# Kernel tuning notes

Measured on AMD Instinct MI355X. Metric: run time of the kernel, lower is better.

Reference implementation:

```python
import jax, jax.numpy as jnp
import numpy as np

G = 8            # grid_size
G2 = G * G       # total_grid_size = 64
NS = 2.0         # neighborhood_size
H = 64           # h_dim
A = 1024         # bottleneck_dim == attention_dim
S = 32           # number of sequences
N = 64           # pedestrians per sequence
P = 4096         # scene boundary points per sequence (down_samples)
B = S * N        # total batch = 2048


def setup_inputs() -> dict:
    key = jax.random.key(0)
    ks = jax.random.split(key, 16)
    starts = jnp.arange(S, dtype=jnp.int32) * N
    seq_start_end = jnp.stack([starts, starts + N], axis=1)  # (S, 2) uniform groups
    return {
        "h_states": jax.random.normal(ks[0], (1, B, H), jnp.float32),
        "end_pos": jax.random.normal(ks[1], (B, 2), jnp.float32),
        "rel_pos": jax.random.normal(ks[2], (B, 2), jnp.float32) * 0.1,
        "scene_info": jax.random.normal(ks[3], (S, P, 2), jnp.float32),
        # Attention_Decoder params (soft attention over G2 grid cells, encoder_dim=1)
        "W_enc": jax.random.normal(ks[4], (1, A), jnp.float32) * 0.05,
        "b_enc": jnp.zeros((A,), jnp.float32),
        "W_dec": jax.random.normal(ks[5], (H, A), jnp.float32) * 0.05,
        "b_dec": jnp.zeros((A,), jnp.float32),
        "w_full": jax.random.normal(ks[6], (A, 1), jnp.float32) * 0.05,
        "b_full": jnp.zeros((1,), jnp.float32),
        "W_out": jax.random.normal(ks[7], (1 + H + 4, A), jnp.float32) * 0.05,  # [ctx, h, embed_info]
        "b_out": jnp.zeros((A,), jnp.float32),
        # mlp_pool: Linear(A, A) + BatchNorm1d + ReLU
        "W_mlp": jax.random.normal(ks[8], (A, A), jnp.float32) * 0.05,
        "b_mlp": jnp.zeros((A,), jnp.float32),
        "gamma": jnp.ones((A,), jnp.float32),
        "beta": jnp.zeros((A,), jnp.float32),
        "seq_start_end": seq_start_end,
    }


def _occupancy(end_pos, scene_info, num_seqs, peds, grid_size, ns):
    """Vectorized per-pedestrian grid-cell binning + scatter-add occupancy.
    end_pos: (num_seqs*peds, 2), scene_info: (num_seqs, P, 2) -> (B, G2)."""
    g2 = grid_size * grid_size
    b = num_seqs * peds
    ep = end_pos.reshape(num_seqs, peds, 1, 2)
    sx = scene_info[:, None, :, 0]  # (S, 1, P)
    sy = scene_info[:, None, :, 1]
    tl_x = ep[..., 0] - ns / 2
    tl_y = ep[..., 1] + ns / 2
    br_x = ep[..., 0] + ns / 2
    br_y = ep[..., 1] - ns / 2
    cell_x = jnp.floor((sx - tl_x) / ns * grid_size)   # (S, N, P)
    cell_y = jnp.floor((tl_y - sy) / ns * grid_size)
    cell = (cell_x + cell_y * grid_size).astype(jnp.int32)
    # point is out-of-bound if outside the ped's neighborhood box (matches torch mask)
    oob = (sx >= br_x) | (sx <= tl_x) | (sy >= tl_y) | (sy <= br_y)
    ped = jnp.arange(b, dtype=jnp.int32).reshape(num_seqs, peds, 1)
    # torch scatters masked points into slot 0 then drops it; we use one dump slot at the end
    idx = jnp.where(oob, b * g2, ped * g2 + cell)      # (S, N, P)
    counts = jax.ops.segment_sum(
        jnp.ones(idx.size, jnp.float32), idx.reshape(-1), num_segments=b * g2 + 1)
    return counts[:-1].reshape(b, g2)


def reference(h_states, end_pos, rel_pos, scene_info,
              W_enc, b_enc, W_dec, b_dec, w_full, b_full,
              W_out, b_out, W_mlp, b_mlp, gamma, beta, seq_start_end):
    num_seqs = seq_start_end.shape[0]
    b = end_pos.shape[0]
    peds = b // num_seqs
    occ = _occupancy(end_pos, scene_info, num_seqs, peds, G, NS)   # (B, G2)
    enc = occ[..., None]                                           # (B, G2, 1)
    h = h_states.reshape(b, -1)                                    # (B, H)
    embed_info = jnp.concatenate([end_pos, rel_pos], axis=1)       # (B, 4)
    # soft attention over the G2 grid cells conditioned on the decoder hidden state
    att = jax.nn.relu(enc @ W_enc + b_enc + (h @ W_dec + b_dec)[:, None, :])  # (B, G2, A)
    e = (att @ w_full)[..., 0] + b_full                            # (B, G2)
    alpha = jax.nn.softmax(e, axis=1)
    ctx = jnp.sum(alpha[..., None] * enc, axis=1)                  # (B, 1)
    pool = jnp.concatenate([ctx, h, embed_info], axis=1) @ W_out + b_out  # (B, A)
    # mlp_pool: Linear -> BatchNorm1d (training stats, biased var) -> ReLU
    y = pool @ W_mlp + b_mlp
    mu = jnp.mean(y, axis=0)
    var = jnp.mean((y - mu) ** 2, axis=0)
    y = gamma * (y - mu) * jax.lax.rsqrt(var + 1e-5) + beta
    return jax.nn.relu(y)
```

## Files before the change

### kernel.cpp

```cpp
#include <hip/hip_runtime.h>
#include <hip/hip_bf16.h>


#define NG2  64
#define NPTS 4096

typedef unsigned short ushort_t;
typedef __attribute__((ext_vector_type(8))) short bf16x8;
typedef __attribute__((ext_vector_type(4))) float f32x4;

struct PrepPtrs { const void* p[16]; };

__device__ __forceinline__ float bf2f(ushort_t u) {
  return __uint_as_float(((unsigned int)u) << 16);
}
__device__ __forceinline__ ushort_t f2bf(float f) {
  __hip_bfloat16 b = __float2bfloat16(f);
  return *reinterpret_cast<ushort_t*>(&b);
}
__device__ __forceinline__ float lde(const void* p, size_t i, int fl) {
  return fl ? bf2f(((const ushort_t*)p)[i]) : ((const float*)p)[i];
}
__device__ __forceinline__ int block_flag(const ushort_t* h) {
  __shared__ int bad_sh;
  if (threadIdx.x == 0) bad_sh = 0;
  __syncthreads();
  float v = bf2f(h[threadIdx.x & 255]);
  if (!(fabsf(v) <= 1e4f)) atomicOr(&bad_sh, 1);
  __syncthreads();
  return (bad_sh == 0) ? 1 : 0;
}

__device__ __forceinline__ void tp_body(const void* in, int fl, int job,
                                        int Kin, int Kpad, ushort_t* out) {
  __shared__ ushort_t t[32][40];
  int n0 = (job & 31) * 32, k0 = (job >> 5) * 32;
  int r = threadIdx.x >> 3, c4 = (threadIdx.x & 7) * 4;
  ushort4 v = make_ushort4(0, 0, 0, 0);
  if (k0 + r < Kin) {
    size_t off = (size_t)(k0 + r) * 1024 + n0 + c4;
    if (fl) {
      v = *(const ushort4*)((const ushort_t*)in + off);
    } else {
      float4 f = *(const float4*)((const float*)in + off);
      v = make_ushort4(f2bf(f.x), f2bf(f.y), f2bf(f.z), f2bf(f.w));
    }
  }
  *(ushort4*)(&t[r][c4]) = v;
  __syncthreads();
  int n = threadIdx.x >> 3, kk = (threadIdx.x & 7) * 4;
  ushort4 o = make_ushort4(t[kk][n], t[kk + 1][n], t[kk + 2][n], t[kk + 3][n]);
  *(ushort4*)(out + (size_t)(n0 + n) * Kpad + k0 + kk) = o;
}

__global__ __launch_bounds__(256) void k_prep(PrepPtrs ptrs,
                                              float* __restrict__ conv,
                                              ushort_t* __restrict__ hbf,
                                              ushort_t* __restrict__ WdecT,
                                              ushort_t* __restrict__ WoutT,
                                              ushort_t* __restrict__ WmlpT,
                                              ushort_t* __restrict__ Xcat0,
                                              float* __restrict__ occ,
                                              float* __restrict__ stats) {
  int b = blockIdx.x;
  int fl = block_flag((const ushort_t*)ptrs.p[0]);
  if (b < 9) {
    int idx = (b * 256 + threadIdx.x) * 4;
    int seg = idx >> 10, off = idx & 1023;
    float4 o;
    if (fl) {
      const unsigned int* src = (const unsigned int*)ptrs.p[7 + seg];
      uint2 u = *(const uint2*)(src + (off >> 1));
      o.x = __uint_as_float((u.x & 0xFFFFu) << 16);
      o.y = __uint_as_float(u.x & 0xFFFF0000u);
      o.z = __uint_as_float((u.y & 0xFFFFu) << 16);
      o.w = __uint_as_float(u.y & 0xFFFF0000u);
    } else {
      o = *(const float4*)((const float*)ptrs.p[7 + seg] + off);
    }
    *(float4*)(conv + idx) = o;
  } else if (b < 137) {
    int i = (b - 9) * 256 + threadIdx.x;
    if (fl) {
      ((ushort4*)hbf)[i] = ((const ushort4*)ptrs.p[0])[i];
    } else {
      float4 f = ((const float4*)ptrs.p[0])[i];
      ((ushort4*)hbf)[i] = make_ushort4(f2bf(f.x), f2bf(f.y), f2bf(f.z), f2bf(f.w));
    }
  } else if (b < 201) {
    tp_body(ptrs.p[1], fl, b - 137, 64, 64, WdecT);
  } else if (b < 297) {
    const void* wout1 = fl ? (const void*)((const ushort_t*)ptrs.p[2] + 1024)
                           : (const void*)((const float*)ptrs.p[2] + 1024);
    tp_body(wout1, fl, b - 201, 68, 96, WoutT);
  } else if (b < 1321) {
    tp_body(ptrs.p[3], fl, b - 297, 1024, 1024, WmlpT);
  } else if (b < 1513) {
    int flat = (b - 1321) * 256 + threadIdx.x;
    int e4 = flat * 4;
    int r = e4 / 96, c = e4 - r * 96;
    ushort4 v = make_ushort4(0, 0, 0, 0);
    if (c < 64) {
      if (fl) v = *(const ushort4*)((const ushort_t*)ptrs.p[0] + r * 64 + c);
      else {
        float4 f = *(const float4*)((const float*)ptrs.p[0] + r * 64 + c);
        v = make_ushort4(f2bf(f.x), f2bf(f.y), f2bf(f.z), f2bf(f.w));
      }
    } else if (c == 64) {
      v.x = f2bf(lde(ptrs.p[4], 2 * r, fl));
      v.y = f2bf(lde(ptrs.p[4], 2 * r + 1, fl));
      v.z = f2bf(lde(ptrs.p[5], 2 * r, fl));
      v.w = f2bf(lde(ptrs.p[5], 2 * r + 1, fl));
    }
    *(ushort4*)(Xcat0 + e4) = v;
  } else if (b < 3561) {
    int i = b - 1513;
    int s = i >> 6;
    __shared__ float cnth[NG2];
    if (threadIdx.x < NG2) cnth[threadIdx.x] = 0.0f;
    __syncthreads();
    float ex = lde(ptrs.p[4], 2 * i, fl), ey = lde(ptrs.p[4], 2 * i + 1, fl);
    float tlx = ex - 1.0f, tly = ey + 1.0f, brx = ex + 1.0f, bry = ey - 1.0f;
    const void* scn = ptrs.p[6];
    for (int p = threadIdx.x; p < NPTS; p += 256) {
      size_t o2 = (size_t)s * NPTS * 2 + 2 * p;
      float sx = lde(scn, o2, fl), sy = lde(scn, o2 + 1, fl);
      bool oob = (sx >= brx) || (sx <= tlx) || (sy >= tly) || (sy <= bry);
      if (!oob) {
        int cx = (int)floorf((sx - tlx) * 0.5f * 8.0f);
        int cy = (int)floorf((tly - sy) * 0.5f * 8.0f);
        int cell = cx + cy * 8;
        if (cell >= 0 && cell < NG2) atomicAdd(&cnth[cell], 1.0f);
      }
    }
    __syncthreads();
    if (threadIdx.x < NG2) occ[i * NG2 + threadIdx.x] = cnth[threadIdx.x];
  } else {
#pragma unroll
    for (int k = 0; k < 8; k++) stats[threadIdx.x + 256 * k] = 0.0f;
  }
}

template <int K, int EPI>
__device__ __forceinline__ void mgemm_body(
    ushort_t* As, ushort_t* Bs, int m0, int n0,
    const ushort_t* __restrict__ A, int lda,
    const ushort_t* __restrict__ BT, int ldb,
    const float* __restrict__ bias1, const float* __restrict__ bias2,
    ushort_t* __restrict__ outb, float* __restrict__ outf) {
  int tid = threadIdx.x;
  int wave = tid >> 6, lane = tid & 63, l15 = lane & 15, kg = lane >> 4;
  f32x4 acc[4][2] = {};
  int ar = tid >> 2, ag = tid & 3;
  int aswz = ag ^ ((ar >> 1) & 3);
  for (int k0 = 0; k0 < K; k0 += 32) {
    uint4 av = *(const uint4*)(A + (size_t)(m0 + ar) * lda + k0 + ag * 8);
    *(uint4*)(&As[ar * 32 + aswz * 8]) = av;
#pragma unroll
    for (int i = 0; i < 2; i++) {
      int c = tid + i * 256;
      int br = c >> 2, bg = c & 3;
      int bswz = bg ^ ((br >> 1) & 3);
      uint4 bv = *(const uint4*)(BT + (size_t)(n0 + br) * ldb + k0 + bg * 8);
      *(uint4*)(&Bs[br * 32 + bswz * 8]) = bv;
    }
    __syncthreads();
    bf16x8 af[4], bfr[2];
#pragma unroll
    for (int mt = 0; mt < 4; mt++) {
      int row = mt * 16 + l15;
      int swz = kg ^ ((row >> 1) & 3);
      af[mt] = *(const bf16x8*)(&As[row * 32 + swz * 8]);
    }
#pragma unroll
    for (int nt = 0; nt < 2; nt++) {
      int row = wave * 32 + nt * 16 + l15;
      int swz = kg ^ ((row >> 1) & 3);
      bfr[nt] = *(const bf16x8*)(&Bs[row * 32 + swz * 8]);
    }
#pragma unroll
    for (int mt = 0; mt < 4; mt++)
#pragma unroll
      for (int nt = 0; nt < 2; nt++)
        acc[mt][nt] = __builtin_amdgcn_mfma_f32_16x16x32_bf16(af[mt], bfr[nt], acc[mt][nt], 0, 0, 0);
    __syncthreads();
  }
#pragma unroll
  for (int nt = 0; nt < 2; nt++) {
    int col = n0 + wave * 32 + nt * 16 + l15;
    float bsum = (EPI == 0) ? (bias1[col] + bias2[col]) : bias1[col];
#pragma unroll
    for (int mt = 0; mt < 4; mt++) {
#pragma unroll
      for (int r = 0; r < 4; r++) {
        int rowm = m0 + mt * 16 + kg * 4 + r;
        float v = acc[mt][nt][r] + bsum;
        if (EPI == 3) outf[(size_t)rowm * 1024 + col] = v;
        else outb[(size_t)rowm * 1024 + col] = f2bf(v);
      }
    }
  }
}

__global__ __launch_bounds__(256) void k_gemm2(
    const ushort_t* __restrict__ hbf, const ushort_t* __restrict__ WdecT,
    const float* __restrict__ benc, const float* __restrict__ bdec,
    ushort_t* __restrict__ hd_out,
    const ushort_t* __restrict__ Xcat0, const ushort_t* __restrict__ WoutT,
    const float* __restrict__ bout, float* __restrict__ P1) {
  __shared__ ushort_t As[64 * 32];
  __shared__ ushort_t Bs[128 * 32];
  int m0 = blockIdx.x * 64, n0 = blockIdx.y * 128;
  if (blockIdx.z == 0)
    mgemm_body<64, 0>(As, Bs, m0, n0, hbf, 64, WdecT, 64, benc, bdec, hd_out, nullptr);
  else
    mgemm_body<96, 3>(As, Bs, m0, n0, Xcat0, 96, WoutT, 96, bout, nullptr, nullptr, P1);
}

__global__ __launch_bounds__(256) void k_ygemm(
    const ushort_t* __restrict__ A, const ushort_t* __restrict__ BT,
    const float* __restrict__ bias1, ushort_t* __restrict__ outb,
    float* __restrict__ stats) {
  __shared__ ushort_t As[64 * 32];
  __shared__ ushort_t Bs[64 * 32];
  int m0 = blockIdx.x * 64, n0 = blockIdx.y * 64;
  int tid = threadIdx.x;
  int wave = tid >> 6, lane = tid & 63, l15 = lane & 15, kg = lane >> 4;
  f32x4 acc[4] = {};
  int ar = tid >> 2, ag = tid & 3;
  int aswz = ag ^ ((ar >> 1) & 3);
  for (int k0 = 0; k0 < 1024; k0 += 32) {
    uint4 av = *(const uint4*)(A + (size_t)(m0 + ar) * 1024 + k0 + ag * 8);
    *(uint4*)(&As[ar * 32 + aswz * 8]) = av;
    {
      int br = tid >> 2, bg = tid & 3;
      int bswz = bg ^ ((br >> 1) & 3);
      uint4 bv = *(const uint4*)(BT + (size_t)(n0 + br) * 1024 + k0 + bg * 8);
      *(uint4*)(&Bs[br * 32 + bswz * 8]) = bv;
    }
    __syncthreads();
    bf16x8 af[4], bfr;
#pragma unroll
    for (int mt = 0; mt < 4; mt++) {
      int row = mt * 16 + l15;
      int swz = kg ^ ((row >> 1) & 3);
      af[mt] = *(const bf16x8*)(&As[row * 32 + swz * 8]);
    }
    {
      int row = wave * 16 + l15;
      int swz = kg ^ ((row >> 1) & 3);
      bfr = *(const bf16x8*)(&Bs[row * 32 + swz * 8]);
    }
#pragma unroll
    for (int mt = 0; mt < 4; mt++)
      acc[mt] = __builtin_amdgcn_mfma_f32_16x16x32_bf16(af[mt], bfr, acc[mt], 0, 0, 0);
    __syncthreads();
  }
  int col = n0 + wave * 16 + l15;
  float bsum = bias1[col];
  float s1 = 0.0f, s2 = 0.0f;
#pragma unroll
  for (int mt = 0; mt < 4; mt++) {
#pragma unroll
    for (int r = 0; r < 4; r++) {
      int rowm = m0 + mt * 16 + kg * 4 + r;
      float v = acc[mt][r] + bsum;
      outb[(size_t)rowm * 1024 + col] = f2bf(v);
      s1 += v; s2 = fmaf(v, v, s2);
    }
  }
  s1 += __shfl_down(s1, 16); s2 += __shfl_down(s2, 16);
  s1 += __shfl_down(s1, 32); s2 += __shfl_down(s2, 32);
  if (lane < 16) {
    atomicAdd(&stats[col], s1);
    atomicAdd(&stats[1024 + col], s2);
  }
}

__global__ __launch_bounds__(256) void k_ectx(
    const float* __restrict__ occ,
    const float* __restrict__ Wenc, const float* __restrict__ wfull,
    const float* __restrict__ w0, const float* __restrict__ P1,
    const ushort_t* __restrict__ hd, ushort_t* __restrict__ pool) {
  int wave = threadIdx.x >> 6, lane = threadIdx.x & 63;
  int p = blockIdx.x * 4 + wave;
  __shared__ float occ_sh[4][64];
  occ_sh[wave][lane] = occ[p * 64 + lane];
  float hdv[16], we[16], wf[16];
#pragma unroll
  for (int j = 0; j < 16; j++) {
    int a = lane + j * 64;
    hdv[j] = bf2f(hd[(size_t)p * 1024 + a]);
    we[j] = Wenc[a];
    wf[j] = wfull[a];
  }
  float e_mine = 0.0f;
  for (int g = 0; g < 64; g++) {
    float c = occ_sh[wave][g];
    float s = 0.0f;
#pragma unroll
    for (int j = 0; j < 16; j++)
      s += fmaxf(fmaf(c, we[j], hdv[j]), 0.0f) * wf[j];
#pragma unroll
    for (int off = 32; off > 0; off >>= 1) s += __shfl_xor(s, off);
    if (lane == g) e_mine = s;
  }
  float m = e_mine;
#pragma unroll
  for (int off = 32; off > 0; off >>= 1) m = fmaxf(m, __shfl_xor(m, off));
  float xe = __expf(e_mine - m);
  float den = xe;
#pragma unroll
  for (int off = 32; off > 0; off >>= 1) den += __shfl_xor(den, off);
  float cp = xe * occ_sh[wave][lane];
#pragma unroll
  for (int off = 32; off > 0; off >>= 1) cp += __shfl_xor(cp, off);
  float ctx = cp / den;
#pragma unroll
  for (int j = 0; j < 16; j++) {
    int a = lane + j * 64;
    pool[(size_t)p * 1024 + a] = f2bf(fmaf(ctx, w0[a], P1[(size_t)p * 1024 + a]));
  }
}

__global__ void k_norm(const ushort_t* __restrict__ y_mf,
                       const float* __restrict__ stats,
                       const float* __restrict__ gamma, const float* __restrict__ beta,
                       const ushort_t* __restrict__ hsrc, void* __restrict__ out) {
  int fl = block_flag(hsrc);
  int idx = (blockIdx.x * 256 + threadIdx.x) * 4;
  int col = idx & 1023;
  float vv[4];
#pragma unroll
  for (int j = 0; j < 4; j++) vv[j] = bf2f(y_mf[idx + j]);
  float4 s1 = *(const float4*)(stats + col);
  float4 s2 = *(const float4*)(stats + 1024 + col);
  float4 gm = *(const float4*)(gamma + col);
  float4 bt = *(const float4*)(beta + col);
  const float ib = 1.0f / 2048.0f;
  float m1[4] = {s1.x, s1.y, s1.z, s1.w};
  float m2[4] = {s2.x, s2.y, s2.z, s2.w};
  float gg[4] = {gm.x, gm.y, gm.z, gm.w};
  float bb[4] = {bt.x, bt.y, bt.z, bt.w};
  float o[4];
#pragma unroll
  for (int j = 0; j < 4; j++) {
    float mu = m1[j] * ib;
    float var = fmaf(-mu, mu, m2[j] * ib);
    o[j] = fmaxf(fmaf(gg[j] * (vv[j] - mu), rsqrtf(var + 1e-5f), bb[j]), 0.0f);
  }
  if (fl) {
    ushort4 ov = make_ushort4(f2bf(o[0]), f2bf(o[1]), f2bf(o[2]), f2bf(o[3]));
    *(ushort4*)((ushort_t*)out + idx) = ov;
  } else {
    *(float4*)((float*)out + idx) = make_float4(o[0], o[1], o[2], o[3]);
  }
}

extern "C" void kernel_launch(void* const* d_in, const int* in_sizes, int n_in,
                              void* d_out, int out_size, void* d_ws, size_t ws_size,
                              hipStream_t stream) {
  float* ws = (float*)d_ws;
  float* conv   = ws;
  float* c_Wenc = conv + 0;
  float* c_benc = conv + 1024;
  float* c_bdec = conv + 2048;
  float* c_wful = conv + 3072;
  float* c_bout = conv + 4096;
  float* c_bmlp = conv + 5120;
  float* c_gam  = conv + 6144;
  float* c_bet  = conv + 7168;
  float* c_w0   = conv + 8192;
  float* occ    = ws + 9216;
  float* stats  = ws + 140288;
  float* P1     = ws + 142336;
  ushort_t* u0    = (ushort_t*)(ws + 2239488);
  ushort_t* hbf   = u0;
  ushort_t* WdecT = u0 + 131072;
  ushort_t* WoutT = u0 + 196608;
  ushort_t* WmlpT = u0 + 294912;
  ushort_t* Xcat0 = u0 + 1343488;
  ushort_t* y_mf  = u0 + 1540096;
  ushort_t* hd_bf   = (ushort_t*)d_out;
  ushort_t* pool_mf = (ushort_t*)d_out;

  PrepPtrs ptrs;
  ptrs.p[0] = d_in[0];
  ptrs.p[1] = d_in[6];
  ptrs.p[2] = d_in[10];
  ptrs.p[3] = d_in[12];
  ptrs.p[4] = d_in[1];
  ptrs.p[5] = d_in[2];
  ptrs.p[6] = d_in[3];
  ptrs.p[7]  = d_in[4];
  ptrs.p[8]  = d_in[5];
  ptrs.p[9]  = d_in[7];
  ptrs.p[10] = d_in[8];
  ptrs.p[11] = d_in[11];
  ptrs.p[12] = d_in[13];
  ptrs.p[13] = d_in[14];
  ptrs.p[14] = d_in[15];
  ptrs.p[15] = d_in[10];

  k_prep<<<3562, 256, 0, stream>>>(ptrs, conv, hbf, WdecT, WoutT, WmlpT,
                                   Xcat0, occ, stats);

  k_gemm2<<<dim3(32, 8, 2), 256, 0, stream>>>(hbf, WdecT, c_benc, c_bdec, hd_bf,
                                              Xcat0, WoutT, c_bout, P1);

  k_ectx<<<512, 256, 0, stream>>>(occ, c_Wenc, c_wful, c_w0, P1, hd_bf, pool_mf);

  k_ygemm<<<dim3(32, 16), 256, 0, stream>>>(pool_mf, WmlpT, c_bmlp, y_mf, stats);

  k_norm<<<2048, 256, 0, stream>>>(y_mf, stats, c_gam, c_bet,
                                   (const ushort_t*)d_in[0], d_out);
}
```

Before: 162.4 us.

## Rebalance prep kernel: larger per-block work for copy, transpose, and occupancy binning

Shrinks the prep kernel grid from 3562 to 1194 blocks by giving each block more work. The h_states conversion now handles 8 elements per thread. The W_mlp transpose uses dedicated 64x64 LDS tiles with padded rows in place of the generic tp_body. Occupancy binning runs one pedestrian per wavefront with per-wave LDS histograms and vectorized scene-point loads. The aim is to cut block launch and scheduling overhead and get better load widths, at the cost of less parallelism per pedestrian in the binning loop.

```diff
diff --git a/kernel.cpp b/kernel.cpp
--- a/kernel.cpp
+++ b/kernel.cpp
@@ -79,24 +79,52 @@
       o = *(const float4*)((const float*)ptrs.p[7 + seg] + off);
     }
     *(float4*)(conv + idx) = o;
-  } else if (b < 137) {
+  } else if (b < 73) {
     int i = (b - 9) * 256 + threadIdx.x;
     if (fl) {
-      ((ushort4*)hbf)[i] = ((const ushort4*)ptrs.p[0])[i];
+      ((uint4*)hbf)[i] = ((const uint4*)ptrs.p[0])[i];
     } else {
-      float4 f = ((const float4*)ptrs.p[0])[i];
-      ((ushort4*)hbf)[i] = make_ushort4(f2bf(f.x), f2bf(f.y), f2bf(f.z), f2bf(f.w));
-    }
-  } else if (b < 201) {
-    tp_body(ptrs.p[1], fl, b - 137, 64, 64, WdecT);
-  } else if (b < 297) {
+      float4 f0 = ((const float4*)ptrs.p[0])[2 * i];
+      float4 f1 = ((const float4*)ptrs.p[0])[2 * i + 1];
+      ((ushort4*)hbf)[2 * i]     = make_ushort4(f2bf(f0.x), f2bf(f0.y), f2bf(f0.z), f2bf(f0.w));
+      ((ushort4*)hbf)[2 * i + 1] = make_ushort4(f2bf(f1.x), f2bf(f1.y), f2bf(f1.z), f2bf(f1.w));
+    }
+  } else if (b < 137) {
+    tp_body(ptrs.p[1], fl, b - 73, 64, 64, WdecT);
+  } else if (b < 233) {
     const void* wout1 = fl ? (const void*)((const ushort_t*)ptrs.p[2] + 1024)
                            : (const void*)((const float*)ptrs.p[2] + 1024);
-    tp_body(wout1, fl, b - 201, 68, 96, WoutT);
-  } else if (b < 1321) {
-    tp_body(ptrs.p[3], fl, b - 297, 1024, 1024, WmlpT);
-  } else if (b < 1513) {
-    int flat = (b - 1321) * 256 + threadIdx.x;
+    tp_body(wout1, fl, b - 137, 68, 96, WoutT);
+  } else if (b < 489) {
+    __shared__ ushort_t t64[64 * 68];
+    int job = b - 233;
+    int n0 = (job & 15) * 64, k0 = (job >> 4) * 64;
+    const void* in = ptrs.p[3];
+#pragma unroll
+    for (int i = 0; i < 4; i++) {
+      int chunk = threadIdx.x + i * 256;
+      int r = chunk >> 4, c4 = (chunk & 15) * 4;
+      ushort4 v;
+      size_t off = (size_t)(k0 + r) * 1024 + n0 + c4;
+      if (fl) {
+        v = *(const ushort4*)((const ushort_t*)in + off);
+      } else {
+        float4 f = *(const float4*)((const float*)in + off);
+        v = make_ushort4(f2bf(f.x), f2bf(f.y), f2bf(f.z), f2bf(f.w));
+      }
+      *(ushort4*)(&t64[r * 68 + c4]) = v;
+    }
+    __syncthreads();
+#pragma unroll
+    for (int i = 0; i < 4; i++) {
+      int chunk = threadIdx.x + i * 256;
+      int n = chunk >> 4, k4 = (chunk & 15) * 4;
+      ushort4 o = make_ushort4(t64[(k4 + 0) * 68 + n], t64[(k4 + 1) * 68 + n],
+                               t64[(k4 + 2) * 68 + n], t64[(k4 + 3) * 68 + n]);
+      *(ushort4*)(WmlpT + (size_t)(n0 + n) * 1024 + k0 + k4) = o;
+    }
+  } else if (b < 681) {
+    int flat = (b - 489) * 256 + threadIdx.x;
     int e4 = flat * 4;
     int r = e4 / 96, c = e4 - r * 96;
     ushort4 v = make_ushort4(0, 0, 0, 0);
@@ -113,28 +141,37 @@
       v.w = f2bf(lde(ptrs.p[5], 2 * r + 1, fl));
     }
     *(ushort4*)(Xcat0 + e4) = v;
-  } else if (b < 3561) {
-    int i = b - 1513;
+  } else if (b < 1193) {
+    int wave = threadIdx.x >> 6, lane = threadIdx.x & 63;
+    int i = (b - 681) * 4 + wave;
     int s = i >> 6;
-    __shared__ float cnth[NG2];
-    if (threadIdx.x < NG2) cnth[threadIdx.x] = 0.0f;
+    __shared__ float cnth[4][NG2];
+    cnth[wave][lane] = 0.0f;
     __syncthreads();
     float ex = lde(ptrs.p[4], 2 * i, fl), ey = lde(ptrs.p[4], 2 * i + 1, fl);
     float tlx = ex - 1.0f, tly = ey + 1.0f, brx = ex + 1.0f, bry = ey - 1.0f;
     const void* scn = ptrs.p[6];
-    for (int p = threadIdx.x; p < NPTS; p += 256) {
-      size_t o2 = (size_t)s * NPTS * 2 + 2 * p;
-      float sx = lde(scn, o2, fl), sy = lde(scn, o2 + 1, fl);
+    for (int p = lane; p < NPTS; p += 64) {
+      size_t pi = (size_t)s * NPTS + p;
+      float sx, sy;
+      if (fl) {
+        unsigned int u = ((const unsigned int*)scn)[pi];
+        sx = __uint_as_float((u & 0xFFFFu) << 16);
+        sy = __uint_as_float(u & 0xFFFF0000u);
+      } else {
+        float2 f = *((const float2*)scn + pi);
+        sx = f.x; sy = f.y;
+      }
       bool oob = (sx >= brx) || (sx <= tlx) || (sy >= tly) || (sy <= bry);
       if (!oob) {
         int cx = (int)floorf((sx - tlx) * 0.5f * 8.0f);
         int cy = (int)floorf((tly - sy) * 0.5f * 8.0f);
         int cell = cx + cy * 8;
-        if (cell >= 0 && cell < NG2) atomicAdd(&cnth[cell], 1.0f);
+        if (cell >= 0 && cell < NG2) atomicAdd(&cnth[wave][cell], 1.0f);
       }
     }
     __syncthreads();
-    if (threadIdx.x < NG2) occ[i * NG2 + threadIdx.x] = cnth[threadIdx.x];
+    occ[(size_t)i * NG2 + lane] = cnth[wave][lane];
   } else {
 #pragma unroll
     for (int k = 0; k < 8; k++) stats[threadIdx.x + 256 * k] = 0.0f;
@@ -402,7 +439,7 @@
   ptrs.p[14] = d_in[15];
   ptrs.p[15] = d_in[10];
 
-  k_prep<<<3562, 256, 0, stream>>>(ptrs, conv, hbf, WdecT, WoutT, WmlpT,
+  k_prep<<<1194, 256, 0, stream>>>(ptrs, conv, hbf, WdecT, WoutT, WmlpT,
                                    Xcat0, occ, stats);
 
   k_gemm2<<<dim3(32, 8, 2), 256, 0, stream>>>(hbf, WdecT, c_benc, c_bdec, hd_bf,
```

New measurement: 167.4 us. 3.1% more time.
